# Performance work log

Measured on AMD Instinct MI355X. Metric: run time of the kernel, lower is better.

Reference implementation:

```python
import jax, jax.numpy as jnp
import numpy as np

B = 262144
IN, H = 2, 50


def setup_inputs() -> dict:
    key = jax.random.key(0)
    ks = jax.random.split(key, 12)
    k = 1.0 / np.sqrt(H)
    u = lambda kk, shape: jax.random.uniform(kk, shape, jnp.float32, -k, k)
    return {
        "s": jax.random.normal(ks[0], (B, IN), jnp.float32),
        "h": jax.random.normal(ks[1], (B, H), jnp.float32),
        "w_ih": u(ks[2], (3 * H, IN)),
        "w_hh": u(ks[3], (3 * H, H)),
        "b_ih": u(ks[4], (3 * H,)),
        "b_hh": u(ks[5], (3 * H,)),
        "actor_w": u(ks[6], (2, H)),
        "actor_b": u(ks[7], (2,)),
        "critic_w": u(ks[8], (1, H)),
        "critic_b": u(ks[9], (1,)),
    }


def reference(s, h, w_ih, w_hh, b_ih, b_hh, actor_w, actor_b, critic_w, critic_b):
    # PyTorch GRUCell gate math (gate order: reset, update, new)
    gi = s @ w_ih.T + b_ih          # [B, 3H]
    gh = h @ w_hh.T + b_hh          # [B, 3H]
    i_r, i_z, i_n = jnp.split(gi, 3, axis=1)
    h_r, h_z, h_n = jnp.split(gh, 3, axis=1)
    r = jax.nn.sigmoid(i_r + h_r)
    z = jax.nn.sigmoid(i_z + h_z)
    n = jnp.tanh(i_n + r * h_n)
    h_new = (1.0 - z) * n + z * h   # [B, H]
    c = h_new @ critic_w.T + critic_b            # [B, 1]
    pi = jax.nn.softmax(h_new @ actor_w.T + actor_b, axis=1)  # [B, 2]
    return h_new, c, pi
```

## Files before the change

kernel.cpp:

```cpp
#include <hip/hip_runtime.h>
#include <hip/hip_bf16.h>


#define BDIM 256

typedef __bf16 bf16x8 __attribute__((ext_vector_type(8)));
typedef float f32x4 __attribute__((ext_vector_type(4)));
typedef unsigned u32x4 __attribute__((ext_vector_type(4)));
typedef unsigned __attribute__((may_alias)) u32a;
typedef unsigned short __attribute__((may_alias)) u16a;

__device__ __forceinline__ float bf2f(unsigned short u) {
    union { unsigned u; float f; } x; x.u = ((unsigned)u) << 16; return x.f;
}
__device__ __forceinline__ unsigned short f2bf(float f) {
    union { float f; unsigned u; } x; x.f = f;
    unsigned r = x.u + 0x7fffu + ((x.u >> 16) & 1u);
    return (unsigned short)(r >> 16);
}
__device__ __forceinline__ unsigned packbf(float a, float b) {
    union { __hip_bfloat162 h; unsigned u; } c;
    c.h = __float22bfloat162_rn(make_float2(a, b));
    return c.u;
}
__device__ __forceinline__ bf16x8 ldsfrag(const unsigned short* p) {
    bf16x8 v; __builtin_memcpy(&v, p, 16); return v;
}

template <int CTRL>
__device__ __forceinline__ float dpp_add(float v) {
    int s = __builtin_bit_cast(int, v);
    int r = __builtin_amdgcn_update_dpp(s, s, CTRL, 0xf, 0xf, false);
    return v + __builtin_bit_cast(float, r);
}
__device__ __forceinline__ float row16_sum(float v) {
    v = dpp_add<0x128>(v);
    v = dpp_add<0x124>(v);
    v = dpp_add<0x122>(v);
    v = dpp_add<0x121>(v);
    return v;
}

__global__ __launch_bounds__(256, 1) void pack_w(
    const float* __restrict__ w_ih, const float* __restrict__ w_hh,
    const float* __restrict__ b_ih, const float* __restrict__ b_hh,
    u32x4* __restrict__ ws)
{
    int e = blockIdx.x * 256 + threadIdx.x;
    if (e >= 1536) return;
    int ln = e & 63;
    int ks = (e >> 6) & 1;
    int t  = (e >> 7) & 3;
    int g  = e >> 9;
    int n  = t * 16 + (ln & 15);
    int kbase = ks * 32 + (ln >> 4) * 8;
    unsigned short vals[8];
    if (n < 50) {
        int r = g * 50 + n;
        #pragma unroll
        for (int i = 0; i < 8; ++i) {
            int k = kbase + i;
            float v = 0.f;
            if (k < 50)       v = w_hh[r * 50 + k];
            else if (k == 50) v = (g < 2) ? w_ih[r * 2 + 0] : 0.f;
            else if (k == 51) v = (g < 2) ? w_ih[r * 2 + 1] : 0.f;
            else if (k == 52) {
                v = b_hh[r];
                if (g < 2) v += b_ih[r];
            }
            vals[i] = f2bf(v);
        }
    } else {
        #pragma unroll
        for (int i = 0; i < 8; ++i) vals[i] = 0;
    }
    u32x4 o;
    #pragma unroll
    for (int i = 0; i < 4; ++i)
        o[i] = (unsigned)vals[2 * i] | ((unsigned)vals[2 * i + 1] << 16);
    ws[e] = o;
}

__global__ __launch_bounds__(BDIM, 2) void gru_fused(
    const float* __restrict__ s,
    const float* __restrict__ h,
    const float* __restrict__ w_ih,
    const float* __restrict__ actor_w,
    const float* __restrict__ actor_b,
    const float* __restrict__ critic_w,
    const float* __restrict__ critic_b,
    const float* __restrict__ b_ih,
    const u32x4* __restrict__ ws,
    float* __restrict__ out,
    int Btot, int nTiles)
{
    __shared__ __align__(16) unsigned short xlds[64 * 72];

    const int tid  = threadIdx.x;
    const int wave = tid >> 6;
    const int lane = tid & 63;
    const int c16  = lane & 15;
    const int quad = lane >> 4;
    const int R    = wave * 16;

    u32a* xlds32 = (u32a*)xlds;

    for (int i = lane; i < 160; i += 64) {
        int row = R + i / 10, dk = 26 + i % 10;
        xlds32[row * 36 + dk] = (i % 10 == 0) ? 0x00003f80u : 0u;
    }
    asm volatile("" ::: "memory");

    bf16x8 wf[3][4][2];
    #pragma unroll
    for (int g = 0; g < 3; ++g)
        #pragma unroll
        for (int t = 0; t < 4; ++t)
            #pragma unroll
            for (int ks = 0; ks < 2; ++ks) {
                u32x4 w = ws[(g << 9) + (t << 7) + (ks << 6) + lane];
                asm volatile("" :: "v"(w));
                wf[g][t][ks] = __builtin_bit_cast(bf16x8, w);
            }

    float wi0[4], wi1[4], bi[4], aw0[4], aw1[4], awc[4];
    #pragma unroll
    for (int t = 0; t < 4; ++t) {
        int j = t * 16 + c16;
        bool ok = (j < 50);
        wi0[t] = ok ? w_ih[(100 + j) * 2 + 0] : 0.f;
        wi1[t] = ok ? w_ih[(100 + j) * 2 + 1] : 0.f;
        bi[t]  = ok ? b_ih[100 + j]           : 0.f;
        aw0[t] = ok ? actor_w[j]              : 0.f;
        aw1[t] = ok ? actor_w[50 + j]         : 0.f;
        awc[t] = ok ? critic_w[j]             : 0.f;
    }
    const float ab0 = actor_b[0], ab1 = actor_b[1], cb = critic_b[0];

    const float2* h2 = (const float2*)h;
    const float2* s2 = (const float2*)s;
    float* oc = out + (long long)Btot * 50;
    float2* opi = (float2*)(out + (long long)Btot * 51);

    float2 pf[7];
    int bt = blockIdx.x;
    {
        long long hb = (long long)(bt * 64 + R) * 25;
        #pragma unroll
        for (int j = 0; j < 6; ++j) pf[j] = h2[hb + lane + j * 64];
        if (lane < 16)      pf[6] = h2[hb + 384 + lane];
        else if (lane < 32) pf[6] = s2[bt * 64 + R + lane - 16];
    }

    while (bt < nTiles) {
        const int rowbase = bt * 64;

        #pragma unroll
        for (int j = 0; j < 6; ++j) {
            int d = lane + j * 64;
            int r = d / 25, dk = d - r * 25;
            xlds32[(R + r) * 36 + dk] = packbf(pf[j].x, pf[j].y);
        }
        if (lane < 16)
            xlds32[(R + 15) * 36 + 9 + lane] = packbf(pf[6].x, pf[6].y);
        else if (lane < 32)
            xlds32[(R + lane - 16) * 36 + 25] = packbf(pf[6].x, pf[6].y);

        asm volatile("" ::: "memory");

        const int nbt = bt + gridDim.x;
        {
            int pb = (nbt < nTiles) ? nbt : bt;
            long long hb = (long long)(pb * 64 + R) * 25;
            #pragma unroll
            for (int j = 0; j < 6; ++j) pf[j] = h2[hb + lane + j * 64];
            if (lane < 16)      pf[6] = h2[hb + 384 + lane];
            else if (lane < 32) pf[6] = s2[pb * 64 + R + lane - 16];
        }

        float2 srow[4];
        #pragma unroll
        for (int reg = 0; reg < 4; ++reg)
            srow[reg] = s2[rowbase + R + quad * 4 + reg];

        const unsigned short* arow = &xlds[(R + c16) * 72 + quad * 8];
        bf16x8 a0 = ldsfrag(arow);
        bf16x8 a1 = ldsfrag(arow + 32);

        float* ob = out + (long long)rowbase * 50;

        float hn_r[4][4];
        #pragma unroll
        for (int t = 0; t < 4; ++t) {
            f32x4 ar = {0.f,0.f,0.f,0.f}, az = ar, an = ar;
            ar = __builtin_amdgcn_mfma_f32_16x16x32_bf16(a0, wf[0][t][0], ar, 0, 0, 0);
            ar = __builtin_amdgcn_mfma_f32_16x16x32_bf16(a1, wf[0][t][1], ar, 0, 0, 0);
            az = __builtin_amdgcn_mfma_f32_16x16x32_bf16(a0, wf[1][t][0], az, 0, 0, 0);
            az = __builtin_amdgcn_mfma_f32_16x16x32_bf16(a1, wf[1][t][1], az, 0, 0, 0);
            an = __builtin_amdgcn_mfma_f32_16x16x32_bf16(a0, wf[2][t][0], an, 0, 0, 0);
            an = __builtin_amdgcn_mfma_f32_16x16x32_bf16(a1, wf[2][t][1], an, 0, 0, 0);

            int j = t * 16 + c16;
            #pragma unroll
            for (int reg = 0; reg < 4; ++reg) {
                int lr = R + quad * 4 + reg;
                float inn = fmaf(srow[reg].y, wi1[t],
                            fmaf(srow[reg].x, wi0[t], bi[t]));
                float rg = __builtin_amdgcn_rcpf(1.f + __expf(-ar[reg]));
                float zg = __builtin_amdgcn_rcpf(1.f + __expf(-az[reg]));
                float x = inn + rg * an[reg];
                float e2 = __expf(2.f * x);
                float ng = 1.f - 2.f * __builtin_amdgcn_rcpf(e2 + 1.f);
                float hv = bf2f(((const u16a*)xlds)[lr * 72 + j]);
                float hnew = fmaf(zg, hv - ng, ng);
                hn_r[reg][t] = (j < 50) ? hnew : 0.f;
                if (j < 50) ob[lr * 50 + j] = hnew;
            }
        }

        float sum0[4], sum1[4], sumc[4];
        #pragma unroll
        for (int reg = 0; reg < 4; ++reg) {
            float p0 = 0.f, p1 = 0.f, pc = 0.f;
            #pragma unroll
            for (int t = 0; t < 4; ++t) {
                p0 = fmaf(hn_r[reg][t], aw0[t], p0);
                p1 = fmaf(hn_r[reg][t], aw1[t], p1);
                pc = fmaf(hn_r[reg][t], awc[t], pc);
            }
            sum0[reg] = row16_sum(p0);
            sum1[reg] = row16_sum(p1);
            sumc[reg] = row16_sum(pc);
        }
        if (c16 < 4) {
            float A0 = (c16 == 0) ? sum0[0] : (c16 == 1) ? sum0[1]
                     : (c16 == 2) ? sum0[2] : sum0[3];
            float A1 = (c16 == 0) ? sum1[0] : (c16 == 1) ? sum1[1]
                     : (c16 == 2) ? sum1[2] : sum1[3];
            float C  = (c16 == 0) ? sumc[0] : (c16 == 1) ? sumc[1]
                     : (c16 == 2) ? sumc[2] : sumc[3];
            int gr = rowbase + R + quad * 4 + c16;
            oc[gr] = C + cb;
            A0 += ab0; A1 += ab1;
            float m = fmaxf(A0, A1);
            float e0 = __expf(A0 - m), e1 = __expf(A1 - m);
            float inv = 1.f / (e0 + e1);
            float2 pv; pv.x = e0 * inv; pv.y = e1 * inv;
            opi[gr] = pv;
        }
        bt = nbt;
    }
}

extern "C" void kernel_launch(void* const* d_in, const int* in_sizes, int n_in,
                              void* d_out, int out_size, void* d_ws, size_t ws_size,
                              hipStream_t stream) {
    const float* s        = (const float*)d_in[0];
    const float* h        = (const float*)d_in[1];
    const float* w_ih     = (const float*)d_in[2];
    const float* w_hh     = (const float*)d_in[3];
    const float* b_ih     = (const float*)d_in[4];
    const float* b_hh     = (const float*)d_in[5];
    const float* actor_w  = (const float*)d_in[6];
    const float* actor_b  = (const float*)d_in[7];
    const float* critic_w = (const float*)d_in[8];
    const float* critic_b = (const float*)d_in[9];
    float* out = (float*)d_out;

    int Btot = in_sizes[1] / 50;
    int nTiles = Btot / 64;
    int grid = nTiles < 1024 ? nTiles : 1024;

    u32x4* ws = (u32x4*)d_ws;

    pack_w<<<6, 256, 0, stream>>>(w_ih, w_hh, b_ih, b_hh, ws);
    gru_fused<<<grid, BDIM, 0, stream>>>(s, h, w_ih, actor_w, actor_b,
                                         critic_w, critic_b, b_ih,
                                         (const u32x4*)ws, out, Btot, nTiles);
}
```

Measured before the change: 149.6 us.

## Replace persistent grid-stride loop with one-tile-per-block launch and LDS-staged weights

Drops the persistent 1024-block loop with register-resident weight fragments and software prefetch. Each 512-thread block now handles one 128-row tile, copies the packed weight fragments into shared memory once, and reads them per MFMA from LDS. This frees many VGPRs so more waves can be resident (launch bounds raised to 4) and relies on occupancy rather than explicit prefetch to hide memory latency. In exchange, every block re-copies the weights to LDS, adds LDS read traffic per tile, and launches 2048 blocks.

Result: faster. 139.4 us (-6.8%).

```diff
diff --git a/kernel.cpp b/kernel.cpp
--- a/kernel.cpp
+++ b/kernel.cpp
@@ -2,7 +2,7 @@
 #include <hip/hip_bf16.h>
 
 
-#define BDIM 256
+#define BDIM 512
 
 typedef __bf16 bf16x8 __attribute__((ext_vector_type(8)));
 typedef float f32x4 __attribute__((ext_vector_type(4)));
@@ -81,7 +81,7 @@
     ws[e] = o;
 }
 
-__global__ __launch_bounds__(BDIM, 2) void gru_fused(
+__global__ __launch_bounds__(BDIM, 4) void gru_fused(
     const float* __restrict__ s,
     const float* __restrict__ h,
     const float* __restrict__ w_ih,
@@ -94,7 +94,8 @@
     float* __restrict__ out,
     int Btot, int nTiles)
 {
-    __shared__ __align__(16) unsigned short xlds[64 * 72];
+    __shared__ __align__(16) unsigned short xlds[128 * 72];
+    __shared__ __align__(16) unsigned short wlds[1536 * 8];
 
     const int tid  = threadIdx.x;
     const int wave = tid >> 6;
@@ -105,23 +106,28 @@
 
     u32a* xlds32 = (u32a*)xlds;
 
+    const int bt = blockIdx.x;
+    const int rowbase = bt * 128;
+    const float2* h2 = (const float2*)h;
+    const float2* s2 = (const float2*)s;
+
+    float2 pf[7];
+    {
+        long long hb = (long long)(rowbase + R) * 25;
+        #pragma unroll
+        for (int j = 0; j < 6; ++j) pf[j] = h2[hb + lane + j * 64];
+        if (lane < 16)      pf[6] = h2[hb + 384 + lane];
+        else if (lane < 32) pf[6] = s2[rowbase + R + lane - 16];
+    }
+
+    u32x4* wlds16 = (u32x4*)wlds;
+    for (int i = tid; i < 1536; i += BDIM)
+        wlds16[i] = ws[i];
+
     for (int i = lane; i < 160; i += 64) {
         int row = R + i / 10, dk = 26 + i % 10;
         xlds32[row * 36 + dk] = (i % 10 == 0) ? 0x00003f80u : 0u;
     }
-    asm volatile("" ::: "memory");
-
-    bf16x8 wf[3][4][2];
-    #pragma unroll
-    for (int g = 0; g < 3; ++g)
-        #pragma unroll
-        for (int t = 0; t < 4; ++t)
-            #pragma unroll
-            for (int ks = 0; ks < 2; ++ks) {
-                u32x4 w = ws[(g << 9) + (t << 7) + (ks << 6) + lane];
-                asm volatile("" :: "v"(w));
-                wf[g][t][ks] = __builtin_bit_cast(bf16x8, w);
-            }
 
     float wi0[4], wi1[4], bi[4], aw0[4], aw1[4], awc[4];
     #pragma unroll
@@ -137,118 +143,99 @@
     }
     const float ab0 = actor_b[0], ab1 = actor_b[1], cb = critic_b[0];
 
-    const float2* h2 = (const float2*)h;
-    const float2* s2 = (const float2*)s;
+    __syncthreads();
+
+    #pragma unroll
+    for (int j = 0; j < 6; ++j) {
+        int d = lane + j * 64;
+        int r = d / 25, dk = d - r * 25;
+        xlds32[(R + r) * 36 + dk] = packbf(pf[j].x, pf[j].y);
+    }
+    if (lane < 16)
+        xlds32[(R + 15) * 36 + 9 + lane] = packbf(pf[6].x, pf[6].y);
+    else if (lane < 32)
+        xlds32[(R + lane - 16) * 36 + 25] = packbf(pf[6].x, pf[6].y);
+
+    asm volatile("" ::: "memory");
+
+    float2 srow[4];
+    #pragma unroll
+    for (int reg = 0; reg < 4; ++reg)
+        srow[reg] = s2[rowbase + R + quad * 4 + reg];
+
+    const unsigned short* arow = &xlds[(R + c16) * 72 + quad * 8];
+    bf16x8 a0 = ldsfrag(arow);
+    bf16x8 a1 = ldsfrag(arow + 32);
+
+    float* ob = out + (long long)rowbase * 50;
     float* oc = out + (long long)Btot * 50;
     float2* opi = (float2*)(out + (long long)Btot * 51);
 
-    float2 pf[7];
-    int bt = blockIdx.x;
-    {
-        long long hb = (long long)(bt * 64 + R) * 25;
-        #pragma unroll
-        for (int j = 0; j < 6; ++j) pf[j] = h2[hb + lane + j * 64];
-        if (lane < 16)      pf[6] = h2[hb + 384 + lane];
-        else if (lane < 32) pf[6] = s2[bt * 64 + R + lane - 16];
-    }
-
-    while (bt < nTiles) {
-        const int rowbase = bt * 64;
-
-        #pragma unroll
-        for (int j = 0; j < 6; ++j) {
-            int d = lane + j * 64;
-            int r = d / 25, dk = d - r * 25;
-            xlds32[(R + r) * 36 + dk] = packbf(pf[j].x, pf[j].y);
+    float hn_r[4][4];
+    #pragma unroll
+    for (int t = 0; t < 4; ++t) {
+        f32x4 ar = {0.f,0.f,0.f,0.f}, az = ar, an = ar;
+        const int tb = (t * 128 + lane) * 8;
+        bf16x8 br0 = ldsfrag(&wlds[tb]);
+        bf16x8 br1 = ldsfrag(&wlds[tb + 512]);
+        bf16x8 bz0 = ldsfrag(&wlds[tb + 4096]);
+        bf16x8 bz1 = ldsfrag(&wlds[tb + 4608]);
+        bf16x8 bn0 = ldsfrag(&wlds[tb + 8192]);
+        bf16x8 bn1 = ldsfrag(&wlds[tb + 8704]);
+        ar = __builtin_amdgcn_mfma_f32_16x16x32_bf16(a0, br0, ar, 0, 0, 0);
+        ar = __builtin_amdgcn_mfma_f32_16x16x32_bf16(a1, br1, ar, 0, 0, 0);
+        az = __builtin_amdgcn_mfma_f32_16x16x32_bf16(a0, bz0, az, 0, 0, 0);
+        az = __builtin_amdgcn_mfma_f32_16x16x32_bf16(a1, bz1, az, 0, 0, 0);
+        an = __builtin_amdgcn_mfma_f32_16x16x32_bf16(a0, bn0, an, 0, 0, 0);
+        an = __builtin_amdgcn_mfma_f32_16x16x32_bf16(a1, bn1, an, 0, 0, 0);
+
+        int j = t * 16 + c16;
+        #pragma unroll
+        for (int reg = 0; reg < 4; ++reg) {
+            int lr = R + quad * 4 + reg;
+            float inn = fmaf(srow[reg].y, wi1[t],
+                        fmaf(srow[reg].x, wi0[t], bi[t]));
+            float rg = __builtin_amdgcn_rcpf(1.f + __expf(-ar[reg]));
+            float zg = __builtin_amdgcn_rcpf(1.f + __expf(-az[reg]));
+            float x = inn + rg * an[reg];
+            float e2 = __expf(2.f * x);
+            float ng = 1.f - 2.f * __builtin_amdgcn_rcpf(e2 + 1.f);
+            float hv = bf2f(((const u16a*)xlds)[lr * 72 + j]);
+            float hnew = fmaf(zg, hv - ng, ng);
+            hn_r[reg][t] = (j < 50) ? hnew : 0.f;
+            if (j < 50) ob[lr * 50 + j] = hnew;
         }
-        if (lane < 16)
-            xlds32[(R + 15) * 36 + 9 + lane] = packbf(pf[6].x, pf[6].y);
-        else if (lane < 32)
-            xlds32[(R + lane - 16) * 36 + 25] = packbf(pf[6].x, pf[6].y);
-
-        asm volatile("" ::: "memory");
-
-        const int nbt = bt + gridDim.x;
-        {
-            int pb = (nbt < nTiles) ? nbt : bt;
-            long long hb = (long long)(pb * 64 + R) * 25;
-            #pragma unroll
-            for (int j = 0; j < 6; ++j) pf[j] = h2[hb + lane + j * 64];
-            if (lane < 16)      pf[6] = h2[hb + 384 + lane];
-            else if (lane < 32) pf[6] = s2[pb * 64 + R + lane - 16];
+    }
+
+    float sum0[4], sum1[4], sumc[4];
+    #pragma unroll
+    for (int reg = 0; reg < 4; ++reg) {
+        float p0 = 0.f, p1 = 0.f, pc = 0.f;
+        #pragma unroll
+        for (int t = 0; t < 4; ++t) {
+            p0 = fmaf(hn_r[reg][t], aw0[t], p0);
+            p1 = fmaf(hn_r[reg][t], aw1[t], p1);
+            pc = fmaf(hn_r[reg][t], awc[t], pc);
         }
-
-        float2 srow[4];
-        #pragma unroll
-        for (int reg = 0; reg < 4; ++reg)
-            srow[reg] = s2[rowbase + R + quad * 4 + reg];
-
-        const unsigned short* arow = &xlds[(R + c16) * 72 + quad * 8];
-        bf16x8 a0 = ldsfrag(arow);
-        bf16x8 a1 = ldsfrag(arow + 32);
-
-        float* ob = out + (long long)rowbase * 50;
-
-        float hn_r[4][4];
-        #pragma unroll
-        for (int t = 0; t < 4; ++t) {
-            f32x4 ar = {0.f,0.f,0.f,0.f}, az = ar, an = ar;
-            ar = __builtin_amdgcn_mfma_f32_16x16x32_bf16(a0, wf[0][t][0], ar, 0, 0, 0);
-            ar = __builtin_amdgcn_mfma_f32_16x16x32_bf16(a1, wf[0][t][1], ar, 0, 0, 0);
-            az = __builtin_amdgcn_mfma_f32_16x16x32_bf16(a0, wf[1][t][0], az, 0, 0, 0);
-            az = __builtin_amdgcn_mfma_f32_16x16x32_bf16(a1, wf[1][t][1], az, 0, 0, 0);
-            an = __builtin_amdgcn_mfma_f32_16x16x32_bf16(a0, wf[2][t][0], an, 0, 0, 0);
-            an = __builtin_amdgcn_mfma_f32_16x16x32_bf16(a1, wf[2][t][1], an, 0, 0, 0);
-
-            int j = t * 16 + c16;
-            #pragma unroll
-            for (int reg = 0; reg < 4; ++reg) {
-                int lr = R + quad * 4 + reg;
-                float inn = fmaf(srow[reg].y, wi1[t],
-                            fmaf(srow[reg].x, wi0[t], bi[t]));
-                float rg = __builtin_amdgcn_rcpf(1.f + __expf(-ar[reg]));
-                float zg = __builtin_amdgcn_rcpf(1.f + __expf(-az[reg]));
-                float x = inn + rg * an[reg];
-                float e2 = __expf(2.f * x);
-                float ng = 1.f - 2.f * __builtin_amdgcn_rcpf(e2 + 1.f);
-                float hv = bf2f(((const u16a*)xlds)[lr * 72 + j]);
-                float hnew = fmaf(zg, hv - ng, ng);
-                hn_r[reg][t] = (j < 50) ? hnew : 0.f;
-                if (j < 50) ob[lr * 50 + j] = hnew;
-            }
-        }
-
-        float sum0[4], sum1[4], sumc[4];
-        #pragma unroll
-        for (int reg = 0; reg < 4; ++reg) {
-            float p0 = 0.f, p1 = 0.f, pc = 0.f;
-            #pragma unroll
-            for (int t = 0; t < 4; ++t) {
-                p0 = fmaf(hn_r[reg][t], aw0[t], p0);
-                p1 = fmaf(hn_r[reg][t], aw1[t], p1);
-                pc = fmaf(hn_r[reg][t], awc[t], pc);
-            }
-            sum0[reg] = row16_sum(p0);
-            sum1[reg] = row16_sum(p1);
-            sumc[reg] = row16_sum(pc);
-        }
-        if (c16 < 4) {
-            float A0 = (c16 == 0) ? sum0[0] : (c16 == 1) ? sum0[1]
-                     : (c16 == 2) ? sum0[2] : sum0[3];
-            float A1 = (c16 == 0) ? sum1[0] : (c16 == 1) ? sum1[1]
-                     : (c16 == 2) ? sum1[2] : sum1[3];
-            float C  = (c16 == 0) ? sumc[0] : (c16 == 1) ? sumc[1]
-                     : (c16 == 2) ? sumc[2] : sumc[3];
-            int gr = rowbase + R + quad * 4 + c16;
-            oc[gr] = C + cb;
-            A0 += ab0; A1 += ab1;
-            float m = fmaxf(A0, A1);
-            float e0 = __expf(A0 - m), e1 = __expf(A1 - m);
-            float inv = 1.f / (e0 + e1);
-            float2 pv; pv.x = e0 * inv; pv.y = e1 * inv;
-            opi[gr] = pv;
-        }
-        bt = nbt;
+        sum0[reg] = row16_sum(p0);
+        sum1[reg] = row16_sum(p1);
+        sumc[reg] = row16_sum(pc);
+    }
+    if (c16 < 4) {
+        float A0 = (c16 == 0) ? sum0[0] : (c16 == 1) ? sum0[1]
+                 : (c16 == 2) ? sum0[2] : sum0[3];
+        float A1 = (c16 == 0) ? sum1[0] : (c16 == 1) ? sum1[1]
+                 : (c16 == 2) ? sum1[2] : sum1[3];
+        float C  = (c16 == 0) ? sumc[0] : (c16 == 1) ? sumc[1]
+                 : (c16 == 2) ? sumc[2] : sumc[3];
+        int gr = rowbase + R + quad * 4 + c16;
+        oc[gr] = C + cb;
+        A0 += ab0; A1 += ab1;
+        float m = fmaxf(A0, A1);
+        float e0 = __expf(A0 - m), e1 = __expf(A1 - m);
+        float inv = 1.f / (e0 + e1);
+        float2 pv; pv.x = e0 * inv; pv.y = e1 * inv;
+        opi[gr] = pv;
     }
 }
 
@@ -268,13 +255,12 @@
     float* out = (float*)d_out;
 
     int Btot = in_sizes[1] / 50;
-    int nTiles = Btot / 64;
-    int grid = nTiles < 1024 ? nTiles : 1024;
+    int nTiles = Btot / 128;
 
     u32x4* ws = (u32x4*)d_ws;
 
     pack_w<<<6, 256, 0, stream>>>(w_ih, w_hh, b_ih, b_hh, ws);
-    gru_fused<<<grid, BDIM, 0, stream>>>(s, h, w_ih, actor_w, actor_b,
-                                         critic_w, critic_b, b_ih,
-                                         (const u32x4*)ws, out, Btot, nTiles);
-}
+    gru_fused<<<nTiles, BDIM, 0, stream>>>(s, h, w_ih, actor_w, actor_b,
+                                           critic_w, critic_b, b_ih,
+                                           (const u32x4*)ws, out, Btot, nTiles);
+}
```
